# Optimization experiments

Measured on AMD Instinct MI355X. Metric: run time of the kernel, lower is better.

## Reference

```python
import jax, jax.numpy as jnp
import numpy as np

D_MODEL = 1024
N_HEADS = 16
HEAD_DIM = D_MODEL // N_HEADS
B, S = 4, 2048


def setup_inputs() -> dict:
    key = jax.random.key(0)
    ks = jax.random.split(key, 12)
    scale = 1.0 / np.sqrt(D_MODEL)
    inp = {
        "query": jax.random.normal(ks[0], (B, S, D_MODEL), dtype=jnp.float32),
        "key": jax.random.normal(ks[1], (B, S, D_MODEL), dtype=jnp.float32),
        "value": jax.random.normal(ks[2], (B, S, D_MODEL), dtype=jnp.float32),
        "mask": jnp.ones((B, 1, S), dtype=jnp.int32),
        "Wq": jax.random.normal(ks[3], (D_MODEL, D_MODEL), dtype=jnp.float32) * scale,
        "bq": jnp.zeros((D_MODEL,), dtype=jnp.float32),
        "Wk": jax.random.normal(ks[4], (D_MODEL, D_MODEL), dtype=jnp.float32) * scale,
        "bk": jnp.zeros((D_MODEL,), dtype=jnp.float32),
        "Wv": jax.random.normal(ks[5], (D_MODEL, D_MODEL), dtype=jnp.float32) * scale,
        "bv": jnp.zeros((D_MODEL,), dtype=jnp.float32),
        "Wo": jax.random.normal(ks[6], (D_MODEL, D_MODEL), dtype=jnp.float32) * scale,
        "bo": jnp.zeros((D_MODEL,), dtype=jnp.float32),
    }
    return inp


def reference(query, key, value, mask, Wq, bq, Wk, bk, Wv, bv, Wo, bo):
    bsz = query.shape[0]
    # Linear projections (torch nn.Linear: x @ W.T + b), split into heads -> [b, h, s, d]
    def proj(x, W, b):
        y = jnp.einsum("bse,de->bsd", x, W) + b
        return y.reshape(bsz, -1, N_HEADS, HEAD_DIM).transpose(0, 2, 1, 3)

    q = proj(query, Wq, bq)
    k = proj(key, Wk, bk)
    v = proj(value, Wv, bv)

    # NOTE: faithful to source — scale by 1/sqrt(d_model), not 1/sqrt(head_dim)
    scores = jnp.einsum("bhqd,bhkd->bhqk", q, k) / jnp.sqrt(jnp.asarray(D_MODEL, q.dtype))
    # mask [b, 1, s_k] -> unsqueeze(1) -> [b, 1, 1, s_k]; fill -inf where mask == 0
    m = mask[:, None, :, :]
    scores = jnp.where(m == 0, jnp.asarray(-jnp.inf, scores.dtype), scores)
    p_attn = jax.nn.softmax(scores, axis=-1)
    ctx = jnp.einsum("bhqk,bhkd->bhqd", p_attn, v)

    concat = ctx.transpose(0, 2, 1, 3).reshape(bsz, -1, D_MODEL)
    out = jnp.einsum("bse,de->bsd", concat, Wo) + bo
    return out
```

## Files before the change

kernel.cpp:

```cpp
#include <hip/hip_runtime.h>
#include <hip/hip_bf16.h>

typedef unsigned short u16;
typedef __attribute__((ext_vector_type(4))) short short4v;
typedef __attribute__((ext_vector_type(8))) short short8;
typedef __attribute__((ext_vector_type(4))) float float4v;
typedef __attribute__((ext_vector_type(16))) float f32x16;

__device__ __forceinline__ void async_copy16(const void* g, void* l) {
  __builtin_amdgcn_global_load_lds(
      (const __attribute__((address_space(1))) unsigned int*)g,
      (__attribute__((address_space(3))) unsigned int*)l,
      16, 0, 0);
}

__device__ __forceinline__ u16 f2bf(float f) {
  __hip_bfloat16 h = __float2bfloat16(f);
  return *reinterpret_cast<u16*>(&h);
}

__device__ __forceinline__ unsigned pack2(float a, float b) {
  return (unsigned)f2bf(a) | ((unsigned)f2bf(b) << 16);
}

struct CArgs {
  const float* in[7];
  u16* out[7];
  int n[7];
};

__global__ void conv_bf16(CArgs a) {
  int t = blockIdx.y;
  int n = a.n[t];
  long i = ((long)blockIdx.x * blockDim.x + threadIdx.x) * 8;
  if (i >= n) return;
  const float4v* f = (const float4v*)(a.in[t] + i);
  float4v lo = f[0], hi = f[1];
  u16 o[8];
  o[0] = f2bf(lo.x); o[1] = f2bf(lo.y); o[2] = f2bf(lo.z); o[3] = f2bf(lo.w);
  o[4] = f2bf(hi.x); o[5] = f2bf(hi.y); o[6] = f2bf(hi.z); o[7] = f2bf(hi.w);
  *(short8*)(a.out[t] + i) = *(const short8*)o;
}

template <bool OUT_F32>
__device__ __forceinline__
void gemm_body(const u16* __restrict__ A, const u16* __restrict__ W,
               const float* __restrict__ bias, void* __restrict__ Cp,
               int M, int N, int K, int mode) {
  __shared__ __attribute__((aligned(16))) u16 As[128 * 32];
  __shared__ __attribute__((aligned(16))) u16 Ws[128 * 32];

  const int tid  = threadIdx.x;
  const int lane = tid & 63;
  const int wave = tid >> 6;
  const int ln15 = lane & 15;
  const int quad = lane >> 4;
  const int m0 = blockIdx.y * 128;
  const int n0 = blockIdx.x * 128;
  const int wm = (wave & 1) * 64;
  const int wn = (wave >> 1) * 64;

  float4v acc[4][4];
#pragma unroll
  for (int i = 0; i < 4; i++)
#pragma unroll
    for (int j = 0; j < 4; j++) acc[i][j] = (float4v)0.0f;

  for (int k0 = 0; k0 < K; k0 += 32) {
#pragma unroll
    for (int c = 0; c < 2; c++) {
      int e = (c * 256 + tid) * 8;
      int r = e >> 5, col = e & 31;
      async_copy16(A + (size_t)(m0 + r) * K + k0 + col, (void*)(As + e));
      async_copy16(W + (size_t)(n0 + r) * K + k0 + col, (void*)(Ws + e));
    }
    __syncthreads();

    short8 af[4], bfr[4];
#pragma unroll
    for (int i = 0; i < 4; i++)
      af[i] = *(const short8*)(As + (wm + i * 16 + ln15) * 32 + quad * 8);
#pragma unroll
    for (int j = 0; j < 4; j++)
      bfr[j] = *(const short8*)(Ws + (wn + j * 16 + ln15) * 32 + quad * 8);
#pragma unroll
    for (int i = 0; i < 4; i++)
#pragma unroll
      for (int j = 0; j < 4; j++)
        acc[i][j] = __builtin_amdgcn_mfma_f32_16x16x32_bf16(af[i], bfr[j], acc[i][j], 0, 0, 0);
    __syncthreads();
  }

#pragma unroll
  for (int j = 0; j < 4; j++) {
    int n = n0 + wn + j * 16 + ln15;
    float bval = bias[n];
#pragma unroll
    for (int i = 0; i < 4; i++) {
#pragma unroll
      for (int r = 0; r < 4; r++) {
        int m = m0 + wm + i * 16 + quad * 4 + r;
        float v = acc[i][j][r] + bval;
        size_t addr;
        if (mode == 0) {
          addr = (size_t)m * N + n;
        } else {
          int b = m >> 11, s = m & 2047;
          int h = n >> 6, dh = n & 63;
          if (mode == 1) addr = (((size_t)(b * 16 + h)) * 2048 + s) * 64 + dh;
          else           addr = (((size_t)(b * 16 + h)) * 64 + dh) * 2048 + s;
        }
        if (OUT_F32) ((float*)Cp)[addr] = v;
        else         ((u16*)Cp)[addr] = f2bf(v);
      }
    }
  }
}

template <bool OUT_F32>
__global__ __launch_bounds__(256, 2)
void gemm_bt(const u16* __restrict__ A, const u16* __restrict__ W,
             const float* __restrict__ bias, void* __restrict__ Cp,
             int M, int N, int K, int mode) {
  gemm_body<OUT_F32>(A, W, bias, Cp, M, N, K, mode);
}

struct G3 {
  const u16* A[3]; const u16* W[3]; const float* bias[3];
  void* C[3]; int mode[3];
};

__global__ __launch_bounds__(256, 2)
void gemm_qkv(G3 g) {
  const int z = blockIdx.z;
  gemm_body<false>(g.A[z], g.W[z], g.bias[z], g.C[z], 8192, 1024, 1024, g.mode[z]);
}

#define SWZ(c, r) ((c) ^ (((r) & 7) << 3))
__global__ __launch_bounds__(256, 3)
void attn(const u16* __restrict__ Q, const u16* __restrict__ K,
          const u16* __restrict__ Vt, const int* __restrict__ mask,
          u16* __restrict__ Ct) {
  __shared__ __attribute__((aligned(16))) u16 Ks[2][64 * 64];
  __shared__ __attribute__((aligned(16))) u16 Vs[2][64 * 64];

  const int tid  = threadIdx.x;
  const int lane = tid & 63;
  const int wave = tid >> 6;
  const int ln31 = lane & 31;
  const int hi   = lane >> 5;
  const int bh = blockIdx.y;
  const int b = bh >> 4, h = bh & 15;
  const int q0 = blockIdx.x * 128;
  const int qr0 = wave * 32;

  const u16* Qg = Q + ((size_t)bh * 2048 + q0 + qr0) * 64;
  const u16* Kg = K + (size_t)bh * 2048 * 64;
  const u16* Vg = Vt + (size_t)bh * 64 * 2048;
  const int* mg = mask + b * 2048;

  short8 qf[4];
#pragma unroll
  for (int m = 0; m < 4; m++)
    qf[m] = *(const short8*)(Qg + (size_t)ln31 * 64 + m * 16 + hi * 8);

#pragma unroll
  for (int c = 0; c < 2; c++) {
    int e = (c * 256 + tid) * 8;
    int r = e >> 6, col = e & 63;
    int sc = SWZ(col, r);
    *(short8*)(Ks[0] + r * 64 + sc) = *(const short8*)(Kg + (size_t)r * 64 + col);
    *(short8*)(Vs[0] + r * 64 + sc) = *(const short8*)(Vg + (size_t)r * 2048 + col);
  }

  f32x16 acc[2];
#pragma unroll
  for (int d = 0; d < 2; d++) acc[d] = (f32x16)0.0f;
  float lrow = 0.0f;

  for (int t = 0; t < 32; t++) {
    const int buf = t & 1;
    __syncthreads();

    short8 kreg[2], vreg[2];
    const bool havenext = (t + 1) < 32;
    if (havenext) {
      int kt2 = (t + 1) * 64;
#pragma unroll
      for (int c = 0; c < 2; c++) {
        int e = (c * 256 + tid) * 8;
        int r = e >> 6, col = e & 63;
        kreg[c] = *(const short8*)(Kg + (size_t)(kt2 + r) * 64 + col);
        vreg[c] = *(const short8*)(Vg + (size_t)r * 2048 + kt2 + col);
      }
    }

    unsigned bw[2][2][4];
#pragma unroll
    for (int kb = 0; kb < 2; kb++) {
      f32x16 s = (f32x16)0.0f;
#pragma unroll
      for (int m = 0; m < 4; m++) {
        const int krow = kb * 32 + ln31;
        short8 kf = *(const short8*)(Ks[buf] + krow * 64 + SWZ(m * 16 + hi * 8, krow));
        s = __builtin_amdgcn_mfma_f32_32x32x16_bf16(kf, qf[m], s, 0, 0, 0);
      }
      unsigned w[8];
#pragma unroll
      for (int g = 0; g < 4; g++) {
        int4 m4 = *(const int4*)(mg + t * 64 + kb * 32 + g * 8 + hi * 4);
        float mb0 = (m4.x == 0) ? -1e30f : 0.0f;
        float mb1 = (m4.y == 0) ? -1e30f : 0.0f;
        float mb2 = (m4.z == 0) ? -1e30f : 0.0f;
        float mb3 = (m4.w == 0) ? -1e30f : 0.0f;
        float p0 = __expf(s[4 * g + 0] * 0.03125f + mb0);
        float p1 = __expf(s[4 * g + 1] * 0.03125f + mb1);
        float p2 = __expf(s[4 * g + 2] * 0.03125f + mb2);
        float p3 = __expf(s[4 * g + 3] * 0.03125f + mb3);
        lrow += (p0 + p1) + (p2 + p3);
        w[2 * g]     = pack2(p0, p1);
        w[2 * g + 1] = pack2(p2, p3);
      }
#pragma unroll
      for (int c = 0; c < 2; c++) {
        auto r0 = __builtin_amdgcn_permlane32_swap(w[c], w[2 + c], false, false);
        bw[kb][0][c]     = r0[0];
        bw[kb][0][2 + c] = r0[1];
        auto r1 = __builtin_amdgcn_permlane32_swap(w[4 + c], w[6 + c], false, false);
        bw[kb][1][c]     = r1[0];
        bw[kb][1][2 + c] = r1[1];
      }
    }

    if (havenext) {
#pragma unroll
      for (int c = 0; c < 2; c++) {
        int e = (c * 256 + tid) * 8;
        int r = e >> 6, col = e & 63;
        int sc = SWZ(col, r);
        *(short8*)(Ks[buf ^ 1] + r * 64 + sc) = kreg[c];
        *(short8*)(Vs[buf ^ 1] + r * 64 + sc) = vreg[c];
      }
    }

#pragma unroll
    for (int d = 0; d < 2; d++) {
#pragma unroll
      for (int kb = 0; kb < 2; kb++) {
#pragma unroll
        for (int mp = 0; mp < 2; mp++) {
          const int vrow = d * 32 + ln31;
          short8 vf = *(const short8*)(Vs[buf] + vrow * 64 +
                                       SWZ(kb * 32 + mp * 16 + hi * 8, vrow));
          union { unsigned w4[4]; short8 s8; } u;
          u.w4[0] = bw[kb][mp][0]; u.w4[1] = bw[kb][mp][1];
          u.w4[2] = bw[kb][mp][2]; u.w4[3] = bw[kb][mp][3];
          acc[d] = __builtin_amdgcn_mfma_f32_32x32x16_bf16(vf, u.s8, acc[d], 0, 0, 0);
        }
      }
    }
  }

  float l = lrow + __shfl_xor(lrow, 32);
  float inv = 1.0f / l;
  const int s = q0 + qr0 + ln31;
  u16* base = Ct + ((size_t)(b * 2048 + s)) * 1024 + h * 64 + hi * 4;
#pragma unroll
  for (int d = 0; d < 2; d++) {
#pragma unroll
    for (int g = 0; g < 4; g++) {
      u16 o[4];
      o[0] = f2bf(acc[d][4 * g + 0] * inv);
      o[1] = f2bf(acc[d][4 * g + 1] * inv);
      o[2] = f2bf(acc[d][4 * g + 2] * inv);
      o[3] = f2bf(acc[d][4 * g + 3] * inv);
      *(short4v*)(base + d * 32 + g * 8) = *(const short4v*)o;
    }
  }
}


extern "C" void kernel_launch(void* const* d_in, const int* in_sizes, int n_in,
                              void* d_out, int out_size, void* d_ws, size_t ws_size,
                              hipStream_t stream) {
  int iq, ik, iv, im, iWq, ibq, iWk, ibk, iWv, ibv, iWo, ibo;
  if (in_sizes[0] == 8388608) {
    iq = 0; ik = 1; iv = 2; im = 3;
    iWq = 4; ibq = 5; iWk = 6; ibk = 7; iWv = 8; ibv = 9; iWo = 10; ibo = 11;
  } else {
    iWk = 0; iWo = 1; iWq = 2; iWv = 3;
    ibk = 4; ibo = 5; ibq = 6; ibv = 7;
    ik = 8; im = 9; iq = 10; iv = 11;
  }
  const float* query = (const float*)d_in[iq];
  const float* key   = (const float*)d_in[ik];
  const float* value = (const float*)d_in[iv];
  const int*   mask  = (const int*)d_in[im];
  const float* Wq = (const float*)d_in[iWq];
  const float* bq = (const float*)d_in[ibq];
  const float* Wk = (const float*)d_in[iWk];
  const float* bk = (const float*)d_in[ibk];
  const float* Wv = (const float*)d_in[iWv];
  const float* bv = (const float*)d_in[ibv];
  const float* Wo = (const float*)d_in[iWo];
  const float* bo = (const float*)d_in[ibo];

  const long U  = 8388608;
  const long Wn = 1048576;
  u16* ws = (u16*)d_ws;
  u16* cq   = ws;
  u16* ck   = cq + U;
  u16* cv   = ck + U;
  u16* cWq  = cv + U;
  u16* cWk  = cWq + Wn;
  u16* cWv  = cWk + Wn;
  u16* cWo  = cWv + Wn;
  u16* qws  = cWo + Wn;
  u16* kws  = qws + U;
  u16* cws  = ck;

  const size_t need_batched = (size_t)(7 * U + 4 * Wn) * sizeof(u16);
  const bool batched = ws_size >= need_batched;
  u16* vtws = batched ? (kws + U) : cq;

  dim3 blk(256);

  CArgs ca;
  ca.in[0] = query; ca.out[0] = cq;  ca.n[0] = (int)U;
  ca.in[1] = key;   ca.out[1] = ck;  ca.n[1] = (int)U;
  ca.in[2] = value; ca.out[2] = cv;  ca.n[2] = (int)U;
  ca.in[3] = Wq;    ca.out[3] = cWq; ca.n[3] = (int)Wn;
  ca.in[4] = Wk;    ca.out[4] = cWk; ca.n[4] = (int)Wn;
  ca.in[5] = Wv;    ca.out[5] = cWv; ca.n[5] = (int)Wn;
  ca.in[6] = Wo;    ca.out[6] = cWo; ca.n[6] = (int)Wn;
  conv_bf16<<<dim3(4096, 7), blk, 0, stream>>>(ca);

  dim3 gproj(8, 64);
  if (batched) {
    G3 g3;
    g3.A[0] = cq; g3.W[0] = cWq; g3.bias[0] = bq; g3.C[0] = qws;  g3.mode[0] = 1;
    g3.A[1] = ck; g3.W[1] = cWk; g3.bias[1] = bk; g3.C[1] = kws;  g3.mode[1] = 1;
    g3.A[2] = cv; g3.W[2] = cWv; g3.bias[2] = bv; g3.C[2] = vtws; g3.mode[2] = 2;
    gemm_qkv<<<dim3(8, 64, 3), blk, 0, stream>>>(g3);
  } else {
    gemm_bt<false><<<gproj, blk, 0, stream>>>(cq, cWq, bq, qws, 8192, 1024, 1024, 1);
    gemm_bt<false><<<gproj, blk, 0, stream>>>(ck, cWk, bk, kws, 8192, 1024, 1024, 1);
    gemm_bt<false><<<gproj, blk, 0, stream>>>(cv, cWv, bv, vtws, 8192, 1024, 1024, 2);
  }
  attn<<<dim3(16, 64), blk, 0, stream>>>(qws, kws, vtws, mask, cws);
  gemm_bt<true><<<gproj, blk, 0, stream>>>(cws, cWo, bo, d_out, 8192, 1024, 1024, 0);
}
```

Before: 437.2 us.

## Split MFMA accumulator chains, use exp2 softmax, set priority, raise GEMM occupancy

The attention kernel now splits both the QK^T and PV MFMA dependency chains into two independent accumulators, so consecutive MFMAs do not wait on each other's results. Softmax uses the hardware exp2 with a folded log2(e)/32 scale in one fma instead of __expf plus a multiply. s_setprio raises wave priority around the MFMA blocks. Separately, the GEMM launch bounds go from 2 to 3 blocks per SM, which may force register spilling in exchange for more resident waves.

```diff
diff --git a/kernel.cpp b/kernel.cpp
--- a/kernel.cpp
+++ b/kernel.cpp
@@ -21,6 +21,10 @@
 
 __device__ __forceinline__ unsigned pack2(float a, float b) {
   return (unsigned)f2bf(a) | ((unsigned)f2bf(b) << 16);
+}
+
+__device__ __forceinline__ float exp2_fast(float x) {
+  return __builtin_amdgcn_exp2f(x);
 }
 
 struct CArgs {
@@ -118,7 +122,7 @@
 }
 
 template <bool OUT_F32>
-__global__ __launch_bounds__(256, 2)
+__global__ __launch_bounds__(256, 3)
 void gemm_bt(const u16* __restrict__ A, const u16* __restrict__ W,
              const float* __restrict__ bias, void* __restrict__ Cp,
              int M, int N, int K, int mode) {
@@ -130,7 +134,7 @@
   void* C[3]; int mode[3];
 };
 
-__global__ __launch_bounds__(256, 2)
+__global__ __launch_bounds__(256, 3)
 void gemm_qkv(G3 g) {
   const int z = blockIdx.z;
   gemm_body<false>(g.A[z], g.W[z], g.bias[z], g.C[z], 8192, 1024, 1024, g.mode[z]);
@@ -159,6 +163,8 @@
   const u16* Vg = Vt + (size_t)bh * 64 * 2048;
   const int* mg = mask + b * 2048;
 
+  const float C2 = 0.04508422f;
+
   short8 qf[4];
 #pragma unroll
   for (int m = 0; m < 4; m++)
@@ -173,9 +179,9 @@
     *(short8*)(Vs[0] + r * 64 + sc) = *(const short8*)(Vg + (size_t)r * 2048 + col);
   }
 
-  f32x16 acc[2];
-#pragma unroll
-  for (int d = 0; d < 2; d++) acc[d] = (f32x16)0.0f;
+  f32x16 accA[2], accB[2];
+#pragma unroll
+  for (int d = 0; d < 2; d++) { accA[d] = (f32x16)0.0f; accB[d] = (f32x16)0.0f; }
   float lrow = 0.0f;
 
   for (int t = 0; t < 32; t++) {
@@ -198,25 +204,31 @@
     unsigned bw[2][2][4];
 #pragma unroll
     for (int kb = 0; kb < 2; kb++) {
-      f32x16 s = (f32x16)0.0f;
-#pragma unroll
-      for (int m = 0; m < 4; m++) {
-        const int krow = kb * 32 + ln31;
-        short8 kf = *(const short8*)(Ks[buf] + krow * 64 + SWZ(m * 16 + hi * 8, krow));
-        s = __builtin_amdgcn_mfma_f32_32x32x16_bf16(kf, qf[m], s, 0, 0, 0);
-      }
+      const int krow = kb * 32 + ln31;
+      short8 kf0 = *(const short8*)(Ks[buf] + krow * 64 + SWZ(0 * 16 + hi * 8, krow));
+      short8 kf1 = *(const short8*)(Ks[buf] + krow * 64 + SWZ(1 * 16 + hi * 8, krow));
+      short8 kf2 = *(const short8*)(Ks[buf] + krow * 64 + SWZ(2 * 16 + hi * 8, krow));
+      short8 kf3 = *(const short8*)(Ks[buf] + krow * 64 + SWZ(3 * 16 + hi * 8, krow));
+      f32x16 sA = (f32x16)0.0f, sB = (f32x16)0.0f;
+      __builtin_amdgcn_s_setprio(1);
+      sA = __builtin_amdgcn_mfma_f32_32x32x16_bf16(kf0, qf[0], sA, 0, 0, 0);
+      sB = __builtin_amdgcn_mfma_f32_32x32x16_bf16(kf1, qf[1], sB, 0, 0, 0);
+      sA = __builtin_amdgcn_mfma_f32_32x32x16_bf16(kf2, qf[2], sA, 0, 0, 0);
+      sB = __builtin_amdgcn_mfma_f32_32x32x16_bf16(kf3, qf[3], sB, 0, 0, 0);
+      __builtin_amdgcn_s_setprio(0);
+      f32x16 s = sA + sB;
       unsigned w[8];
 #pragma unroll
       for (int g = 0; g < 4; g++) {
         int4 m4 = *(const int4*)(mg + t * 64 + kb * 32 + g * 8 + hi * 4);
-        float mb0 = (m4.x == 0) ? -1e30f : 0.0f;
-        float mb1 = (m4.y == 0) ? -1e30f : 0.0f;
-        float mb2 = (m4.z == 0) ? -1e30f : 0.0f;
-        float mb3 = (m4.w == 0) ? -1e30f : 0.0f;
-        float p0 = __expf(s[4 * g + 0] * 0.03125f + mb0);
-        float p1 = __expf(s[4 * g + 1] * 0.03125f + mb1);
-        float p2 = __expf(s[4 * g + 2] * 0.03125f + mb2);
-        float p3 = __expf(s[4 * g + 3] * 0.03125f + mb3);
+        float mb0 = (m4.x == 0) ? -1.5e30f : 0.0f;
+        float mb1 = (m4.y == 0) ? -1.5e30f : 0.0f;
+        float mb2 = (m4.z == 0) ? -1.5e30f : 0.0f;
+        float mb3 = (m4.w == 0) ? -1.5e30f : 0.0f;
+        float p0 = exp2_fast(fmaf(s[4 * g + 0], C2, mb0));
+        float p1 = exp2_fast(fmaf(s[4 * g + 1], C2, mb1));
+        float p2 = exp2_fast(fmaf(s[4 * g + 2], C2, mb2));
+        float p3 = exp2_fast(fmaf(s[4 * g + 3], C2, mb3));
         lrow += (p0 + p1) + (p2 + p3);
         w[2 * g]     = pack2(p0, p1);
         w[2 * g + 1] = pack2(p2, p3);
@@ -243,22 +255,29 @@
       }
     }
 
+    __builtin_amdgcn_s_setprio(1);
 #pragma unroll
     for (int d = 0; d < 2; d++) {
-#pragma unroll
-      for (int kb = 0; kb < 2; kb++) {
-#pragma unroll
-        for (int mp = 0; mp < 2; mp++) {
-          const int vrow = d * 32 + ln31;
-          short8 vf = *(const short8*)(Vs[buf] + vrow * 64 +
-                                       SWZ(kb * 32 + mp * 16 + hi * 8, vrow));
+      const int vrow = d * 32 + ln31;
+#pragma unroll
+      for (int mp = 0; mp < 2; mp++) {
+        {
+          short8 vf = *(const short8*)(Vs[buf] + vrow * 64 + SWZ(0 * 32 + mp * 16 + hi * 8, vrow));
           union { unsigned w4[4]; short8 s8; } u;
-          u.w4[0] = bw[kb][mp][0]; u.w4[1] = bw[kb][mp][1];
-          u.w4[2] = bw[kb][mp][2]; u.w4[3] = bw[kb][mp][3];
-          acc[d] = __builtin_amdgcn_mfma_f32_32x32x16_bf16(vf, u.s8, acc[d], 0, 0, 0);
+          u.w4[0] = bw[0][mp][0]; u.w4[1] = bw[0][mp][1];
+          u.w4[2] = bw[0][mp][2]; u.w4[3] = bw[0][mp][3];
+          accA[d] = __builtin_amdgcn_mfma_f32_32x32x16_bf16(vf, u.s8, accA[d], 0, 0, 0);
         }
-      }
-    }
+        {
+          short8 vf = *(const short8*)(Vs[buf] + vrow * 64 + SWZ(1 * 32 + mp * 16 + hi * 8, vrow));
+          union { unsigned w4[4]; short8 s8; } u;
+          u.w4[0] = bw[1][mp][0]; u.w4[1] = bw[1][mp][1];
+          u.w4[2] = bw[1][mp][2]; u.w4[3] = bw[1][mp][3];
+          accB[d] = __builtin_amdgcn_mfma_f32_32x32x16_bf16(vf, u.s8, accB[d], 0, 0, 0);
+        }
+      }
+    }
+    __builtin_amdgcn_s_setprio(0);
   }
 
   float l = lrow + __shfl_xor(lrow, 32);
@@ -267,13 +286,14 @@
   u16* base = Ct + ((size_t)(b * 2048 + s)) * 1024 + h * 64 + hi * 4;
 #pragma unroll
   for (int d = 0; d < 2; d++) {
+    f32x16 acc = accA[d] + accB[d];
 #pragma unroll
     for (int g = 0; g < 4; g++) {
       u16 o[4];
-      o[0] = f2bf(acc[d][4 * g + 0] * inv);
-      o[1] = f2bf(acc[d][4 * g + 1] * inv);
-      o[2] = f2bf(acc[d][4 * g + 2] * inv);
-      o[3] = f2bf(acc[d][4 * g + 3] * inv);
+      o[0] = f2bf(acc[4 * g + 0] * inv);
+      o[1] = f2bf(acc[4 * g + 1] * inv);
+      o[2] = f2bf(acc[4 * g + 2] * inv);
+      o[3] = f2bf(acc[4 * g + 3] * inv);
       *(short4v*)(base + d * 32 + g * 8) = *(const short4v*)o;
     }
   }
```

Measured after the change: 490.9 us. 1.12x slower.
